# Optimization experiments

Measured on AMD Instinct MI355X. Metric: run time of the kernel, lower is better.

Reference implementation:

```python
import jax, jax.numpy as jnp
import numpy as np

N = 10000      # nodes
DEG = 8        # avg out-degree before symmetrization
B = 2          # batch
T = 8          # time steps
F_IN = 1
HID = 64       # spatial hidden = temporal hidden
K = 2          # power-conv hops


def setup_inputs() -> dict:
    rng = np.random.default_rng(0)
    # random sparse adjacency, symmetrized by concatenating reversed edges
    s0 = rng.integers(0, N, size=N * DEG)
    d0 = rng.integers(0, N, size=N * DEG)
    src = np.concatenate([s0, d0]).astype(np.int32)   # [E], E = 2*N*DEG
    dst = np.concatenate([d0, s0]).astype(np.int32)
    vals = np.ones(src.shape[0], np.float32)
    # symmetric normalization: A_hat = D^{-1/2} A D^{-1/2}
    deg = np.zeros(N, np.float32)
    np.add.at(deg, dst, vals)
    dinv = 1.0 / np.sqrt(np.maximum(deg, 1.0))
    vals = (dinv[src] * dinv[dst] * vals).astype(np.float32)

    key = jax.random.key(0)
    ks = jax.random.split(key, 12)
    sc = 0.05
    return {
        "x": jax.random.normal(ks[0], (B, N, T), jnp.float32),
        "edge_src": jnp.asarray(src),
        "edge_dst": jnp.asarray(dst),
        "edge_val": jnp.asarray(vals),
        # PowerGConvDyn layer 1: F_in -> HID, K+1 power weights
        "W_sp1": jax.random.normal(ks[1], (K + 1, F_IN, HID), jnp.float32) * sc,
        "b_sp1": jnp.zeros((HID,), jnp.float32),
        # PowerGConvDyn layer 2: HID -> HID
        "W_sp2": jax.random.normal(ks[2], (K + 1, HID, HID), jnp.float32) * sc,
        "b_sp2": jnp.zeros((HID,), jnp.float32),
        # GRU (torch layout: gates stacked r,z,n)
        "W_ih": jax.random.normal(ks[3], (3 * HID, HID), jnp.float32) * sc,
        "W_hh": jax.random.normal(ks[4], (3 * HID, HID), jnp.float32) * sc,
        "b_ih": jnp.zeros((3 * HID,), jnp.float32),
        "b_hh": jnp.zeros((3 * HID,), jnp.float32),
        # head
        "W_head": jax.random.normal(ks[5], (HID, 1), jnp.float32) * sc,
        "b_head": jnp.zeros((1,), jnp.float32),
    }


def reference(x, edge_src, edge_dst, edge_val,
              W_sp1, b_sp1, W_sp2, b_sp2,
              W_ih, W_hh, b_ih, b_hh, W_head, b_head):
    Bb, Nn, Tt = x.shape
    # batch all (b,t) slices as columns: [N, B*T, F_in]
    H = x.transpose(1, 0, 2).reshape(Nn, Bb * Tt, 1)

    def spmm(Z):  # A_hat @ Z on node axis; Z: [N, M, F]
        msgs = edge_val[:, None, None] * Z[edge_src]           # [E, M, F]
        return jax.ops.segment_sum(msgs, edge_dst, num_segments=Nn)

    def power_layer(Hin, W, b):  # out = sum_k (A^k H) W_k + b, then ReLU
        out = jnp.einsum('nmf,fo->nmo', Hin, W[0])
        Z = Hin
        for k in range(1, W.shape[0]):
            Z = spmm(Z)
            out = out + jnp.einsum('nmf,fo->nmo', Z, W[k])
        return jax.nn.relu(out + b)

    H = power_layer(H, W_sp1, b_sp1)   # [N, B*T, HID]
    H = power_layer(H, W_sp2, b_sp2)   # [N, B*T, HID]
    C = H.shape[-1]

    # [N, B*T, C] -> [T, B*N, C] sequences for the GRU
    Hs = H.reshape(Nn, Bb, Tt, C).transpose(2, 1, 0, 3).reshape(Tt, Bb * Nn, C)

    Hh = W_hh.shape[1]
    h0 = jnp.zeros((Bb * Nn, Hh), x.dtype)

    def gru_step(h, xt):
        gx = xt @ W_ih.T + b_ih
        gh = h @ W_hh.T + b_hh
        rx, zx, nx = jnp.split(gx, 3, axis=-1)
        rh, zh, nh = jnp.split(gh, 3, axis=-1)
        r = jax.nn.sigmoid(rx + rh)
        z = jax.nn.sigmoid(zx + zh)
        n = jnp.tanh(nx + r * nh)
        h = (1.0 - z) * n + z * h
        return h, None

    h_last, _ = jax.lax.scan(gru_step, h0, Hs)   # [B*N, HID]
    y = (h_last @ W_head + b_head).reshape(Bb, Nn)
    return y
```

## Files before the change

kernel.cpp:

```cpp
#include <hip/hip_runtime.h>
#include <math.h>

#define N_NODES 10000
#define B_SZ 2
#define T_STEPS 8
#define M_COLS 16
#define BN 20000
#define NM 160000

typedef __attribute__((ext_vector_type(8))) short short8;
typedef __attribute__((ext_vector_type(4))) float f32x4;

__device__ __forceinline__ float b2f(unsigned short u) {
  union { unsigned int i; float f; } x; x.i = ((unsigned int)u) << 16; return x.f;
}
__device__ __forceinline__ unsigned short f2b(float f) {
  unsigned int x = __float_as_uint(f);
  return (unsigned short)((x + 0x7fffu + ((x >> 16) & 1u)) >> 16);
}
__device__ __forceinline__ float sigm(float x) {
  return 1.f / (1.f + __expf(-x));
}
__device__ __forceinline__ float tanhfast(float x) {
  float xm = fmaxf(x, -15.f);
  float e = __expf(-2.f * xm);
  return (1.f - e) / (1.f + e);
}

__global__ __launch_bounds__(256) void k_count(const int* __restrict__ dst, int* __restrict__ cnt, int E) {
  int e = blockIdx.x*256 + threadIdx.x;
  if (e < E) atomicAdd(&cnt[dst[e]], 1);
}

__global__ __launch_bounds__(256) void k_scan(const int* __restrict__ cnt, int* __restrict__ rowp, int n) {
  const int K = 40;
  int t = threadIdx.x;
  int beg = t*K;
  int end = beg + K < n ? beg + K : n;
  int s = 0;
  for (int i = beg; i < end; ++i) s += cnt[i];
  int lane = t & 63, w = t >> 6;
  int v = s;
#pragma unroll
  for (int off = 1; off < 64; off <<= 1) {
    int u = __shfl_up(v, off, 64);
    if (lane >= off) v += u;
  }
  __shared__ int wsum[4];
  if (lane == 63) wsum[w] = v;
  __syncthreads();
  int woff = 0;
  for (int i = 0; i < w; ++i) woff += wsum[i];
  int run = woff + v - s;
  for (int i = beg; i < end; ++i) { rowp[i] = run; run += cnt[i]; }
  if (t == 255) rowp[n] = run;
}

__global__ __launch_bounds__(256) void k_fill(const int* __restrict__ src, const int* __restrict__ dst,
                                              const float* __restrict__ val, const int* __restrict__ rowp,
                                              int* __restrict__ cur, int* __restrict__ csrs,
                                              float* __restrict__ csrv, int E) {
  int e = blockIdx.x*256 + threadIdx.x;
  if (e >= E) return;
  int d = dst[e];
  int p = atomicAdd(&cur[d], 1);
  int slot = rowp[d] + p;
  csrs[slot] = src[e];
  csrv[slot] = val[e];
}

__global__ __launch_bounds__(256) void k_prep(const float* __restrict__ Wih, const float* __restrict__ W2,
                                              const float* __restrict__ Whh,
                                              unsigned short* __restrict__ Wbih,
                                              unsigned short* __restrict__ W2t,
                                              unsigned short* __restrict__ Whi,
                                              unsigned short* __restrict__ Wlo) {
  int i = blockIdx.x*256 + threadIdx.x;
  if (i >= 12288) return;
  Wbih[i] = f2b(Wih[i]);
  int p = i >> 12, rem = i & 4095, c = rem >> 6, k = rem & 63;
  W2t[i] = f2b(W2[p*4096 + k*64 + c]);
  float v = Whh[i];
  unsigned short h = f2b(v);
  Whi[i] = h;
  Wlo[i] = f2b(v - b2f(h));
}

__global__ __launch_bounds__(256) void k_x2h(const float* __restrict__ x, float* __restrict__ Z0) {
  int i = blockIdx.x*256 + threadIdx.x;
  if (i >= NM) return;
  int n = i >> 4, m = i & 15;
  int b = m >> 3, t = m & 7;
  Z0[i] = x[b*(N_NODES*T_STEPS) + n*T_STEPS + t];
}

__global__ __launch_bounds__(256) void k_spmm16(const float* __restrict__ Zin, float* __restrict__ Zout,
                                                const int* __restrict__ rowp, const int* __restrict__ csrs,
                                                const float* __restrict__ csrv) {
  int i = blockIdx.x*256 + threadIdx.x;
  if (i >= NM) return;
  int n = i >> 4, m = i & 15;
  int s = rowp[n], e = rowp[n+1];
  float acc = 0.f;
  for (int k = s; k < e; ++k)
    acc = fmaf(csrv[k], Zin[csrs[k]*16 + m], acc);
  Zout[i] = acc;
}

__global__ __launch_bounds__(256) void k_layer1(const float* __restrict__ Z0, const float* __restrict__ Z1,
                                                const float* __restrict__ Z2, const float* __restrict__ W1,
                                                const float* __restrict__ b1, unsigned short* __restrict__ H1b) {
  int i = blockIdx.x*256 + threadIdx.x;
  int c = i & 63, nm = i >> 6;
  float v = fmaf(Z0[nm], W1[c], fmaf(Z1[nm], W1[64+c], fmaf(Z2[nm], W1[128+c], b1[c])));
  H1b[i] = f2b(v > 0.f ? v : 0.f);
}

__global__ __launch_bounds__(256) void k_spmmC(const unsigned short* __restrict__ Zin,
                                               unsigned short* __restrict__ Zout,
                                               const int* __restrict__ rowp, const int* __restrict__ csrs,
                                               const float* __restrict__ csrv) {
  int c = blockIdx.x & 7;
  int grp = blockIdx.x >> 3;
  int n = grp*16 + (threadIdx.x >> 4);
  int l = threadIdx.x & 15;
  int off = c*128 + l*8;
  int s = rowp[n], e = rowp[n+1];
  float acc[8] = {0,0,0,0,0,0,0,0};
  for (int k = s; k < e; ++k) {
    int src = csrs[k];
    float v = csrv[k];
    union { uint4 u; unsigned short s[8]; } z;
    z.u = *(const uint4*)(Zin + (size_t)src*1024 + off);
#pragma unroll
    for (int j = 0; j < 8; ++j) acc[j] = fmaf(v, b2f(z.s[j]), acc[j]);
  }
  union { uint4 u; unsigned short s[8]; } o;
#pragma unroll
  for (int j = 0; j < 8; ++j) o.s[j] = f2b(acc[j]);
  *(uint4*)(Zout + (size_t)n*1024 + off) = o.u;
}

__global__ __launch_bounds__(256) void k_layer2m(const unsigned short* __restrict__ H1b,
                                                 const unsigned short* __restrict__ Z1b,
                                                 const unsigned short* __restrict__ Z2b,
                                                 const unsigned short* __restrict__ Wt,
                                                 const float* __restrict__ b2,
                                                 unsigned short* __restrict__ OUT2b) {
  int wid = blockIdx.x*4 + (threadIdx.x >> 6);
  int lane = threadIdx.x & 63;
  int lr = lane & 15, hi = lane >> 4;
  int rowbase = wid*16;
  const short* A0 = (const short*)H1b + (size_t)(rowbase + lr)*64;
  const short* A1 = (const short*)Z1b + (size_t)(rowbase + lr)*64;
  const short* A2 = (const short*)Z2b + (size_t)(rowbase + lr)*64;
  short8 a[3][2];
  a[0][0] = *(const short8*)(A0 + hi*8); a[0][1] = *(const short8*)(A0 + 32 + hi*8);
  a[1][0] = *(const short8*)(A1 + hi*8); a[1][1] = *(const short8*)(A1 + 32 + hi*8);
  a[2][0] = *(const short8*)(A2 + hi*8); a[2][1] = *(const short8*)(A2 + 32 + hi*8);
  const short* Bp = (const short*)Wt;
  f32x4 acc[4];
#pragma unroll
  for (int ct = 0; ct < 4; ++ct) {
    int col = ct*16 + lr;
    f32x4 c = {0.f, 0.f, 0.f, 0.f};
#pragma unroll
    for (int p = 0; p < 3; ++p) {
      short8 b0 = *(const short8*)(Bp + p*4096 + col*64 + hi*8);
      short8 b1 = *(const short8*)(Bp + p*4096 + col*64 + 32 + hi*8);
      c = __builtin_amdgcn_mfma_f32_16x16x32_bf16(a[p][0], b0, c, 0, 0, 0);
      c = __builtin_amdgcn_mfma_f32_16x16x32_bf16(a[p][1], b1, c, 0, 0, 0);
    }
    acc[ct] = c;
  }
#pragma unroll
  for (int ct = 0; ct < 4; ++ct) {
    int col = ct*16 + lr;
    float bb = b2[col];
#pragma unroll
    for (int r = 0; r < 4; ++r) {
      int nm = rowbase + hi*4 + r;
      int n = nm >> 4, m = nm & 15;
      int bi = m >> 3, t = m & 7;
      float v = acc[ct][r] + bb;
      OUT2b[((size_t)((t*2 + bi)*N_NODES + n))*64 + col] = f2b(v > 0.f ? v : 0.f);
    }
  }
}

__global__ __launch_bounds__(256, 2) void k_gru(const unsigned short* __restrict__ OUT2b,
                                                const unsigned short* __restrict__ Whhi,
                                                const unsigned short* __restrict__ Whlo,
                                                const unsigned short* __restrict__ Wihb,
                                                const float* __restrict__ bih,
                                                const float* __restrict__ bhh,
                                                const float* __restrict__ Whead,
                                                const float* __restrict__ bhead,
                                                float* __restrict__ y) {
  extern __shared__ char smem[];
  uint4* WF = (uint4*)smem;
  float* HSb = (float*)(smem + 49152);
  int tid = threadIdx.x;
  for (int idx = tid; idx < 48*64; idx += 256) {
    int f = idx >> 6, ln = idx & 63;
    int lrr = ln & 15, h4r = ln >> 4;
    int g = (f < 24) ? f : f - 24;
    int ct = g >> 1, kc = g & 1;
    const unsigned short* src = (f < 24) ? Whhi : Whlo;
    WF[idx] = *(const uint4*)(src + (ct*16 + lrr)*64 + kc*32 + h4r*8);
  }
  int w = tid >> 6, lane = tid & 63;
  int lr = lane & 15, h4 = lane >> 4;
  float* hs = HSb + w*(16*68);
  for (int i = lane; i < 16*68; i += 64) hs[i] = 0.f;
  __syncthreads();
  int Wv = blockIdx.x*4 + w;
  if (Wv >= 1250) return;
  int base = Wv*16;
  int row0 = base + lr;
  int b0 = row0 >= N_NODES ? 1 : 0;
  int n0 = row0 - b0*N_NODES;

  const short* Wx = (const short*)Wihb;
  short8 wx[12][2];
#pragma unroll
  for (int ct = 0; ct < 12; ++ct)
#pragma unroll
    for (int kc = 0; kc < 2; ++kc)
      wx[ct][kc] = *(const short8*)(Wx + (ct*16 + lr)*64 + kc*32 + h4*8);

  float cR[4], cZ[4], bNi[4], bNh[4];
#pragma unroll
  for (int cr = 0; cr < 4; ++cr) {
    int col = cr*16 + lr;
    cR[cr]  = bih[col] + bhh[col];
    cZ[cr]  = bih[64+col] + bhh[64+col];
    bNi[cr] = bih[128+col];
    bNh[cr] = bhh[128+col];
  }
  float hreg[4][4];
#pragma unroll
  for (int cr = 0; cr < 4; ++cr)
#pragma unroll
    for (int j = 0; j < 4; ++j) hreg[cr][j] = 0.f;
  const short* O = (const short*)OUT2b;

#pragma unroll 1
  for (int t = 0; t < 8; ++t) {
    short8 ax[2];
    size_t ab0 = ((size_t)((t*2 + b0)*N_NODES + n0))*64;
#pragma unroll
    for (int kc = 0; kc < 2; ++kc)
      ax[kc] = *(const short8*)(O + ab0 + kc*32 + h4*8);
    short8 ahi[2], alo[2];
#pragma unroll
    for (int kc = 0; kc < 2; ++kc) {
      const float* hp = hs + lr*68 + kc*32 + h4*8;
      float4 v0 = *(const float4*)hp;
      float4 v1 = *(const float4*)(hp + 4);
      float hv[8];
      hv[0]=v0.x; hv[1]=v0.y; hv[2]=v0.z; hv[3]=v0.w;
      hv[4]=v1.x; hv[5]=v1.y; hv[6]=v1.z; hv[7]=v1.w;
      union { short8 v; unsigned short s[8]; } uh, ul;
#pragma unroll
      for (int j = 0; j < 8; ++j) {
        unsigned short hb = f2b(hv[j]);
        uh.s[j] = hb;
        ul.s[j] = f2b(hv[j] - b2f(hb));
      }
      ahi[kc] = uh.v; alo[kc] = ul.v;
    }
    f32x4 aR[4], aZ[4], aNx[4], aNh[4];
#pragma unroll
    for (int cr = 0; cr < 4; ++cr) {
      f32x4 zz = {0.f,0.f,0.f,0.f};
      aR[cr] = zz; aZ[cr] = zz; aNx[cr] = zz; aNh[cr] = zz;
    }
#pragma unroll
    for (int ct = 0; ct < 12; ++ct) {
#pragma unroll
      for (int kc = 0; kc < 2; ++kc) {
        short8 bhi = *(const short8*)&WF[(ct*2 + kc)*64 + lane];
        short8 blo = *(const short8*)&WF[(24 + ct*2 + kc)*64 + lane];
        if (ct < 4) {
          aR[ct] = __builtin_amdgcn_mfma_f32_16x16x32_bf16(ax[kc],  wx[ct][kc], aR[ct], 0, 0, 0);
          aR[ct] = __builtin_amdgcn_mfma_f32_16x16x32_bf16(ahi[kc], bhi,        aR[ct], 0, 0, 0);
          aR[ct] = __builtin_amdgcn_mfma_f32_16x16x32_bf16(ahi[kc], blo,        aR[ct], 0, 0, 0);
          aR[ct] = __builtin_amdgcn_mfma_f32_16x16x32_bf16(alo[kc], bhi,        aR[ct], 0, 0, 0);
        } else if (ct < 8) {
          int cc = ct - 4;
          aZ[cc] = __builtin_amdgcn_mfma_f32_16x16x32_bf16(ax[kc],  wx[ct][kc], aZ[cc], 0, 0, 0);
          aZ[cc] = __builtin_amdgcn_mfma_f32_16x16x32_bf16(ahi[kc], bhi,        aZ[cc], 0, 0, 0);
          aZ[cc] = __builtin_amdgcn_mfma_f32_16x16x32_bf16(ahi[kc], blo,        aZ[cc], 0, 0, 0);
          aZ[cc] = __builtin_amdgcn_mfma_f32_16x16x32_bf16(alo[kc], bhi,        aZ[cc], 0, 0, 0);
        } else {
          int cc = ct - 8;
          aNx[cc] = __builtin_amdgcn_mfma_f32_16x16x32_bf16(ax[kc],  wx[ct][kc], aNx[cc], 0, 0, 0);
          aNh[cc] = __builtin_amdgcn_mfma_f32_16x16x32_bf16(ahi[kc], bhi,        aNh[cc], 0, 0, 0);
          aNh[cc] = __builtin_amdgcn_mfma_f32_16x16x32_bf16(ahi[kc], blo,        aNh[cc], 0, 0, 0);
          aNh[cc] = __builtin_amdgcn_mfma_f32_16x16x32_bf16(alo[kc], bhi,        aNh[cc], 0, 0, 0);
        }
      }
    }
#pragma unroll
    for (int cr = 0; cr < 4; ++cr)
#pragma unroll
      for (int j = 0; j < 4; ++j) {
        float r = sigm(aR[cr][j] + cR[cr]);
        float z = sigm(aZ[cr][j] + cZ[cr]);
        float nn = tanhfast(aNx[cr][j] + bNi[cr] + r*(aNh[cr][j] + bNh[cr]));
        float hv = (1.f - z)*nn + z*hreg[cr][j];
        hreg[cr][j] = hv;
        hs[(h4*4 + j)*68 + cr*16 + lr] = hv;
      }
  }
  float wv[4];
#pragma unroll
  for (int cr = 0; cr < 4; ++cr) wv[cr] = Whead[cr*16 + lr];
#pragma unroll
  for (int j = 0; j < 4; ++j) {
    float p = 0.f;
#pragma unroll
    for (int cr = 0; cr < 4; ++cr) p = fmaf(hreg[cr][j], wv[cr], p);
    p += __shfl_xor(p, 1, 64);
    p += __shfl_xor(p, 2, 64);
    p += __shfl_xor(p, 4, 64);
    p += __shfl_xor(p, 8, 64);
    if (lr == 0) y[base + h4*4 + j] = p + bhead[0];
  }
}

extern "C" void kernel_launch(void* const* d_in, const int* in_sizes, int n_in,
                              void* d_out, int out_size, void* d_ws, size_t ws_size,
                              hipStream_t stream) {
  const float* x    = (const float*)d_in[0];
  const int*   esrc = (const int*)d_in[1];
  const int*   edst = (const int*)d_in[2];
  const float* eval = (const float*)d_in[3];
  const float* W1   = (const float*)d_in[4];
  const float* b1   = (const float*)d_in[5];
  const float* W2   = (const float*)d_in[6];
  const float* b2   = (const float*)d_in[7];
  const float* Wih  = (const float*)d_in[8];
  const float* Whh  = (const float*)d_in[9];
  const float* bih  = (const float*)d_in[10];
  const float* bhh  = (const float*)d_in[11];
  const float* Whead= (const float*)d_in[12];
  const float* bhead= (const float*)d_in[13];
  int E = in_sizes[1];
  float* y = (float*)d_out;

  char* wsb = (char*)d_ws;
  unsigned short* H1b   = (unsigned short*)(wsb + 0);
  unsigned short* ZB1   = (unsigned short*)(wsb + 20480000);
  unsigned short* ZB2   = (unsigned short*)(wsb + 40960000);
  unsigned short* OUT2b = (unsigned short*)(wsb + 61440000);
  float* Z0   = (float*)(wsb + 81920000);
  float* Z1   = (float*)(wsb + 82560000);
  float* Z2   = (float*)(wsb + 83200000);
  int*   rowp = (int*)(wsb + 83840000);
  int*   cnt  = (int*)(wsb + 83880064);
  int*   csrs = (int*)(wsb + 83920064);
  float* csrv = (float*)(wsb + 84560064);
  unsigned short* Wbih = (unsigned short*)(wsb + 85200064);
  unsigned short* W2t  = (unsigned short*)(wsb + 85224640);
  unsigned short* Whhi = (unsigned short*)(wsb + 85249280);
  unsigned short* Whlo = (unsigned short*)(wsb + 85273856);

  int eb = (E + 255) / 256;

  hipMemsetAsync(cnt, 0, N_NODES*sizeof(int), stream);
  k_count<<<eb, 256, 0, stream>>>(edst, cnt, E);
  k_scan<<<1, 256, 0, stream>>>(cnt, rowp, N_NODES);
  hipMemsetAsync(cnt, 0, N_NODES*sizeof(int), stream);
  k_fill<<<eb, 256, 0, stream>>>(esrc, edst, eval, rowp, cnt, csrs, csrv, E);
  k_prep<<<48, 256, 0, stream>>>(Wih, W2, Whh, Wbih, W2t, Whhi, Whlo);

  k_x2h<<<625, 256, 0, stream>>>(x, Z0);
  k_spmm16<<<625, 256, 0, stream>>>(Z0, Z1, rowp, csrs, csrv);
  k_spmm16<<<625, 256, 0, stream>>>(Z1, Z2, rowp, csrs, csrv);
  k_layer1<<<40000, 256, 0, stream>>>(Z0, Z1, Z2, W1, b1, H1b);

  k_spmmC<<<5000, 256, 0, stream>>>(H1b, ZB1, rowp, csrs, csrv);
  k_spmmC<<<5000, 256, 0, stream>>>(ZB1, ZB2, rowp, csrs, csrv);
  k_layer2m<<<2500, 256, 0, stream>>>(H1b, ZB1, ZB2, W2t, b2, OUT2b);

  const int gru_lds = 49152 + 4*16*68*4;
  hipFuncSetAttribute((const void*)k_gru, hipFuncAttributeMaxDynamicSharedMemorySize, gru_lds);
  k_gru<<<313, 256, gru_lds, stream>>>(OUT2b, Whhi, Whlo, Wbih, bih, bhh, Whead, bhead, y);
}
```

Baseline: 267.8 us.

## Fuse layer-1 SpMMs with input gather and move GRU input weights to LDS

```diff
diff --git a/kernel.cpp b/kernel.cpp
--- a/kernel.cpp
+++ b/kernel.cpp
@@ -86,34 +86,46 @@
   Wlo[i] = f2b(v - b2f(h));
 }
 
-__global__ __launch_bounds__(256) void k_x2h(const float* __restrict__ x, float* __restrict__ Z0) {
+__global__ __launch_bounds__(256) void k_spmmA(const float* __restrict__ x, float* __restrict__ Z1,
+                                               const int* __restrict__ rowp, const int* __restrict__ csrs,
+                                               const float* __restrict__ csrv) {
   int i = blockIdx.x*256 + threadIdx.x;
-  if (i >= NM) return;
   int n = i >> 4, m = i & 15;
   int b = m >> 3, t = m & 7;
-  Z0[i] = x[b*(N_NODES*T_STEPS) + n*T_STEPS + t];
-}
-
-__global__ __launch_bounds__(256) void k_spmm16(const float* __restrict__ Zin, float* __restrict__ Zout,
-                                                const int* __restrict__ rowp, const int* __restrict__ csrs,
-                                                const float* __restrict__ csrv) {
-  int i = blockIdx.x*256 + threadIdx.x;
-  if (i >= NM) return;
-  int n = i >> 4, m = i & 15;
   int s = rowp[n], e = rowp[n+1];
+  const float* xb = x + b*(N_NODES*T_STEPS) + t;
   float acc = 0.f;
   for (int k = s; k < e; ++k)
-    acc = fmaf(csrv[k], Zin[csrs[k]*16 + m], acc);
-  Zout[i] = acc;
-}
-
-__global__ __launch_bounds__(256) void k_layer1(const float* __restrict__ Z0, const float* __restrict__ Z1,
-                                                const float* __restrict__ Z2, const float* __restrict__ W1,
-                                                const float* __restrict__ b1, unsigned short* __restrict__ H1b) {
+    acc = fmaf(csrv[k], xb[csrs[k]*T_STEPS], acc);
+  Z1[i] = acc;
+}
+
+__global__ __launch_bounds__(256) void k_spmmB_l1(const float* __restrict__ x, const float* __restrict__ Z1,
+                                                  const int* __restrict__ rowp, const int* __restrict__ csrs,
+                                                  const float* __restrict__ csrv,
+                                                  const float* __restrict__ W1, const float* __restrict__ b1,
+                                                  unsigned short* __restrict__ H1b) {
   int i = blockIdx.x*256 + threadIdx.x;
-  int c = i & 63, nm = i >> 6;
-  float v = fmaf(Z0[nm], W1[c], fmaf(Z1[nm], W1[64+c], fmaf(Z2[nm], W1[128+c], b1[c])));
-  H1b[i] = f2b(v > 0.f ? v : 0.f);
+  int n = i >> 4, m = i & 15;
+  int b = m >> 3, t = m & 7;
+  int s = rowp[n], e = rowp[n+1];
+  float z2 = 0.f;
+  for (int k = s; k < e; ++k)
+    z2 = fmaf(csrv[k], Z1[csrs[k]*16 + m], z2);
+  float z0 = x[b*(N_NODES*T_STEPS) + n*T_STEPS + t];
+  float z1 = Z1[i];
+  unsigned short* dst = H1b + (size_t)i*64;
+  union { uint4 v; unsigned short s[8]; } o;
+#pragma unroll
+  for (int g = 0; g < 8; ++g) {
+#pragma unroll
+    for (int j = 0; j < 8; ++j) {
+      int c = g*8 + j;
+      float v = fmaf(z0, W1[c], fmaf(z1, W1[64+c], fmaf(z2, W1[128+c], b1[c])));
+      o.s[j] = f2b(v > 0.f ? v : 0.f);
+    }
+    ((uint4*)dst)[g] = o.v;
+  }
 }
 
 __global__ __launch_bounds__(256) void k_spmmC(const unsigned short* __restrict__ Zin,
@@ -188,7 +200,7 @@
   }
 }
 
-__global__ __launch_bounds__(256, 2) void k_gru(const unsigned short* __restrict__ OUT2b,
+__global__ __launch_bounds__(256, 1) void k_gru(const unsigned short* __restrict__ OUT2b,
                                                 const unsigned short* __restrict__ Whhi,
                                                 const unsigned short* __restrict__ Whlo,
                                                 const unsigned short* __restrict__ Wihb,
@@ -199,14 +211,14 @@
                                                 float* __restrict__ y) {
   extern __shared__ char smem[];
   uint4* WF = (uint4*)smem;
-  float* HSb = (float*)(smem + 49152);
+  float* HSb = (float*)(smem + 73728);
   int tid = threadIdx.x;
-  for (int idx = tid; idx < 48*64; idx += 256) {
+  for (int idx = tid; idx < 72*64; idx += 256) {
     int f = idx >> 6, ln = idx & 63;
     int lrr = ln & 15, h4r = ln >> 4;
-    int g = (f < 24) ? f : f - 24;
+    int g = (f < 24) ? f : ((f < 48) ? f - 24 : f - 48);
     int ct = g >> 1, kc = g & 1;
-    const unsigned short* src = (f < 24) ? Whhi : Whlo;
+    const unsigned short* src = (f < 24) ? Whhi : ((f < 48) ? Whlo : Wihb);
     WF[idx] = *(const uint4*)(src + (ct*16 + lrr)*64 + kc*32 + h4r*8);
   }
   int w = tid >> 6, lane = tid & 63;
@@ -221,14 +233,6 @@
   int b0 = row0 >= N_NODES ? 1 : 0;
   int n0 = row0 - b0*N_NODES;
 
-  const short* Wx = (const short*)Wihb;
-  short8 wx[12][2];
-#pragma unroll
-  for (int ct = 0; ct < 12; ++ct)
-#pragma unroll
-    for (int kc = 0; kc < 2; ++kc)
-      wx[ct][kc] = *(const short8*)(Wx + (ct*16 + lr)*64 + kc*32 + h4*8);
-
   float cR[4], cZ[4], bNi[4], bNh[4];
 #pragma unroll
   for (int cr = 0; cr < 4; ++cr) {
@@ -264,7 +268,7 @@
       union { short8 v; unsigned short s[8]; } uh, ul;
 #pragma unroll
       for (int j = 0; j < 8; ++j) {
-        unsigned short hb = f2b(hv[j]);
+        unsigned short hb = (unsigned short)(__float_as_uint(hv[j]) >> 16);
         uh.s[j] = hb;
         ul.s[j] = f2b(hv[j] - b2f(hb));
       }
@@ -282,23 +286,24 @@
       for (int kc = 0; kc < 2; ++kc) {
         short8 bhi = *(const short8*)&WF[(ct*2 + kc)*64 + lane];
         short8 blo = *(const short8*)&WF[(24 + ct*2 + kc)*64 + lane];
+        short8 bx  = *(const short8*)&WF[(48 + ct*2 + kc)*64 + lane];
         if (ct < 4) {
-          aR[ct] = __builtin_amdgcn_mfma_f32_16x16x32_bf16(ax[kc],  wx[ct][kc], aR[ct], 0, 0, 0);
-          aR[ct] = __builtin_amdgcn_mfma_f32_16x16x32_bf16(ahi[kc], bhi,        aR[ct], 0, 0, 0);
-          aR[ct] = __builtin_amdgcn_mfma_f32_16x16x32_bf16(ahi[kc], blo,        aR[ct], 0, 0, 0);
-          aR[ct] = __builtin_amdgcn_mfma_f32_16x16x32_bf16(alo[kc], bhi,        aR[ct], 0, 0, 0);
+          aR[ct] = __builtin_amdgcn_mfma_f32_16x16x32_bf16(ax[kc],  bx,  aR[ct], 0, 0, 0);
+          aR[ct] = __builtin_amdgcn_mfma_f32_16x16x32_bf16(ahi[kc], bhi, aR[ct], 0, 0, 0);
+          aR[ct] = __builtin_amdgcn_mfma_f32_16x16x32_bf16(ahi[kc], blo, aR[ct], 0, 0, 0);
+          aR[ct] = __builtin_amdgcn_mfma_f32_16x16x32_bf16(alo[kc], bhi, aR[ct], 0, 0, 0);
         } else if (ct < 8) {
           int cc = ct - 4;
-          aZ[cc] = __builtin_amdgcn_mfma_f32_16x16x32_bf16(ax[kc],  wx[ct][kc], aZ[cc], 0, 0, 0);
-          aZ[cc] = __builtin_amdgcn_mfma_f32_16x16x32_bf16(ahi[kc], bhi,        aZ[cc], 0, 0, 0);
-          aZ[cc] = __builtin_amdgcn_mfma_f32_16x16x32_bf16(ahi[kc], blo,        aZ[cc], 0, 0, 0);
-          aZ[cc] = __builtin_amdgcn_mfma_f32_16x16x32_bf16(alo[kc], bhi,        aZ[cc], 0, 0, 0);
+          aZ[cc] = __builtin_amdgcn_mfma_f32_16x16x32_bf16(ax[kc],  bx,  aZ[cc], 0, 0, 0);
+          aZ[cc] = __builtin_amdgcn_mfma_f32_16x16x32_bf16(ahi[kc], bhi, aZ[cc], 0, 0, 0);
+          aZ[cc] = __builtin_amdgcn_mfma_f32_16x16x32_bf16(ahi[kc], blo, aZ[cc], 0, 0, 0);
+          aZ[cc] = __builtin_amdgcn_mfma_f32_16x16x32_bf16(alo[kc], bhi, aZ[cc], 0, 0, 0);
         } else {
           int cc = ct - 8;
-          aNx[cc] = __builtin_amdgcn_mfma_f32_16x16x32_bf16(ax[kc],  wx[ct][kc], aNx[cc], 0, 0, 0);
-          aNh[cc] = __builtin_amdgcn_mfma_f32_16x16x32_bf16(ahi[kc], bhi,        aNh[cc], 0, 0, 0);
-          aNh[cc] = __builtin_amdgcn_mfma_f32_16x16x32_bf16(ahi[kc], blo,        aNh[cc], 0, 0, 0);
-          aNh[cc] = __builtin_amdgcn_mfma_f32_16x16x32_bf16(alo[kc], bhi,        aNh[cc], 0, 0, 0);
+          aNx[cc] = __builtin_amdgcn_mfma_f32_16x16x32_bf16(ax[kc],  bx,  aNx[cc], 0, 0, 0);
+          aNh[cc] = __builtin_amdgcn_mfma_f32_16x16x32_bf16(ahi[kc], bhi, aNh[cc], 0, 0, 0);
+          aNh[cc] = __builtin_amdgcn_mfma_f32_16x16x32_bf16(ahi[kc], blo, aNh[cc], 0, 0, 0);
+          aNh[cc] = __builtin_amdgcn_mfma_f32_16x16x32_bf16(alo[kc], bhi, aNh[cc], 0, 0, 0);
         }
       }
     }
@@ -321,11 +326,10 @@
   for (int j = 0; j < 4; ++j) {
     float p = 0.f;
 #pragma unroll
-    for (int cr = 0; cr < 4; ++cr) p = fmaf(hreg[cr][j], wv[cr], p);
-    p += __shfl_xor(p, 1, 64);
-    p += __shfl_xor(p, 2, 64);
-    p += __shfl_xor(p, 4, 64);
-    p += __shfl_xor(p, 8, 64);
+    for (int cr = 0; cr < 4; ++cr) p = fmaf(hreg[j >= 0 ? cr : 0][j], wv[cr], p);
+#pragma unroll
+    for (int off = 1; off <= 8; off <<= 1)
+      p += __shfl_xor(p, off, 64);
     if (lr == 0) y[base + h4*4 + j] = p + bhead[0];
   }
 }
@@ -355,9 +359,7 @@
   unsigned short* ZB1   = (unsigned short*)(wsb + 20480000);
   unsigned short* ZB2   = (unsigned short*)(wsb + 40960000);
   unsigned short* OUT2b = (unsigned short*)(wsb + 61440000);
-  float* Z0   = (float*)(wsb + 81920000);
   float* Z1   = (float*)(wsb + 82560000);
-  float* Z2   = (float*)(wsb + 83200000);
   int*   rowp = (int*)(wsb + 83840000);
   int*   cnt  = (int*)(wsb + 83880064);
   int*   csrs = (int*)(wsb + 83920064);
@@ -376,16 +378,14 @@
   k_fill<<<eb, 256, 0, stream>>>(esrc, edst, eval, rowp, cnt, csrs, csrv, E);
   k_prep<<<48, 256, 0, stream>>>(Wih, W2, Whh, Wbih, W2t, Whhi, Whlo);
 
-  k_x2h<<<625, 256, 0, stream>>>(x, Z0);
-  k_spmm16<<<625, 256, 0, stream>>>(Z0, Z1, rowp, csrs, csrv);
-  k_spmm16<<<625, 256, 0, stream>>>(Z1, Z2, rowp, csrs, csrv);
-  k_layer1<<<40000, 256, 0, stream>>>(Z0, Z1, Z2, W1, b1, H1b);
+  k_spmmA<<<625, 256, 0, stream>>>(x, Z1, rowp, csrs, csrv);
+  k_spmmB_l1<<<625, 256, 0, stream>>>(x, Z1, rowp, csrs, csrv, W1, b1, H1b);
 
   k_spmmC<<<5000, 256, 0, stream>>>(H1b, ZB1, rowp, csrs, csrv);
   k_spmmC<<<5000, 256, 0, stream>>>(ZB1, ZB2, rowp, csrs, csrv);
   k_layer2m<<<2500, 256, 0, stream>>>(H1b, ZB1, ZB2, W2t, b2, OUT2b);
 
-  const int gru_lds = 49152 + 4*16*68*4;
+  const int gru_lds = 73728 + 4*16*68*4;
   hipFuncSetAttribute((const void*)k_gru, hipFuncAttributeMaxDynamicSharedMemorySize, gru_lds);
   k_gru<<<313, 256, gru_lds, stream>>>(OUT2b, Whhi, Whlo, Wbih, bih, bhh, Whead, bhead, y);
 }
```

Result: no change. 270.5 us (+1.0%).
